# Performance work log

Measured on AMD Instinct MI355X. Metric: run time of the kernel, lower is better.

## Reference

```python
import jax, jax.numpy as jnp
import numpy as np
import math

EPS = 1e-12  # matches F.normalize eps


def _l2_normalize(x):
    # F.normalize(x, p=2, dim=1): x / max(||x||, eps)
    n = jnp.sqrt(jnp.sum(x * x, axis=-1, keepdims=True))
    return x / jnp.maximum(n, EPS)


def setup_inputs() -> dict:
    key = jax.random.key(0)
    k1, k2 = jax.random.split(key)
    B, C, D = 4096, 10000, 1024
    features = jax.random.normal(k1, (B, D), dtype=jnp.float32)
    prototypes = jax.random.normal(k2, (C, D), dtype=jnp.float32)
    distance_scale = jnp.ones((1,), dtype=jnp.float32)
    temperature = jnp.ones((1,), dtype=jnp.float32)
    return {"features": features, "prototypes": prototypes,
            "distance_scale": distance_scale, "temperature": temperature}


def reference(features, prototypes, distance_scale, temperature):
    f = _l2_normalize(features)          # [B, D]
    p = _l2_normalize(prototypes)        # [C, D]
    # ||f - p||^2 = 2 - 2 f.p for unit vectors; clamp tiny negatives from fp error
    sq = jnp.maximum(2.0 - 2.0 * jnp.einsum('bd,cd->bc', f, p), EPS)
    dist = jnp.sqrt(sq) / math.sqrt(2.0)                      # [B, C]
    iso = jnp.abs(distance_scale) * dist                      # [B, C]
    logits = -(iso + jnp.mean(iso, axis=1, keepdims=True))
    return logits / temperature
```

## Files before the change

kernel.cpp:

```cpp
#include <hip/hip_runtime.h>
#include <hip/hip_bf16.h>

typedef __attribute__((ext_vector_type(8))) short short8;
typedef __attribute__((ext_vector_type(4))) float f32x4;

#define GLOBAL_AS __attribute__((address_space(1)))
#define LDS_AS    __attribute__((address_space(3)))

__device__ __forceinline__ void async_ld16(const void* g, void* l) {
    __builtin_amdgcn_global_load_lds((const GLOBAL_AS void*)g, (LDS_AS void*)l, 16, 0, 0);
}

__device__ __forceinline__ unsigned short f2bf(float x) {
    union { __hip_bfloat16 h; unsigned short u; } cv;
    cv.h = __float2bfloat16(x);
    return cv.u;
}

__global__ __launch_bounds__(256) void norm_rows_kernel(
    const float* __restrict__ in, unsigned short* __restrict__ outb, int rows_in)
{
    const int row = blockIdx.x;
    const int tid = threadIdx.x;
    float4 v = make_float4(0.f, 0.f, 0.f, 0.f);
    if (row < rows_in)
        v = reinterpret_cast<const float4*>(in + (size_t)row * 1024)[tid];
    float s = v.x * v.x + v.y * v.y + v.z * v.z + v.w * v.w;
    #pragma unroll
    for (int off = 32; off > 0; off >>= 1) s += __shfl_down(s, off);
    __shared__ float sr[4];
    if ((tid & 63) == 0) sr[tid >> 6] = s;
    __syncthreads();
    const float tot = sr[0] + sr[1] + sr[2] + sr[3];
    const float inv = 1.f / fmaxf(sqrtf(tot), 1e-12f);
    ushort4 o;
    o.x = f2bf(v.x * inv);
    o.y = f2bf(v.y * inv);
    o.z = f2bf(v.z * inv);
    o.w = f2bf(v.w * inv);
    reinterpret_cast<ushort4*>(outb + (size_t)row * 1024)[tid] = o;
}

__global__ __launch_bounds__(256) void zero_f32_kernel(float* __restrict__ p, int n)
{
    const int i = blockIdx.x * 256 + threadIdx.x;
    if (i < n) p[i] = 0.f;
}

__global__ __launch_bounds__(512, 2) void gemm_iso_kernel(
    const unsigned short* __restrict__ A,
    const unsigned short* __restrict__ B,
    float* __restrict__ out,
    float* __restrict__ rowsum,
    const float* __restrict__ ds_ptr,
    int M, int C, int K)
{
    __shared__ __align__(16) char lds[131072];

    const float dsv_raw = ds_ptr[0];

    const int tid  = threadIdx.x;
    const int lane = tid & 63;
    const int wid  = tid >> 6;

    const int nwg  = gridDim.x * gridDim.y;
    const int orig = blockIdx.y * gridDim.x + blockIdx.x;
    const int cpx  = nwg >> 3;
    const int swz  = (orig & 7) * cpx + (orig >> 3);
    const int bx   = swz % gridDim.x;
    const int by   = swz / gridDim.x;
    const int brow = by * 256;
    const int bcol = bx * 256;

    const int lrow8 = lane >> 3;
    const int slotg = (lane & 7) ^ lrow8;
    const size_t kb = (size_t)K * 2;

    const char* pA[4]; const char* pB[4]; int lA[4], lB[4];
    #pragma unroll
    for (int i = 0; i < 4; ++i) {
        const int seg = wid * 4 + i;
        const int r   = seg * 8 + lrow8;
        pA[i] = (const char*)A + (size_t)(brow + r) * kb + slotg * 16;
        pB[i] = (const char*)B + (size_t)(bcol + r) * kb + slotg * 16;
        lA[i] = seg * 1024;
        lB[i] = 32768 + seg * 1024;
    }

    auto STAGE = [&](int buf) {
        char* base = lds + (buf << 16);
        #pragma unroll
        for (int i = 0; i < 4; ++i) async_ld16(pA[i], base + lA[i]);
        #pragma unroll
        for (int i = 0; i < 4; ++i) async_ld16(pB[i], base + lB[i]);
        #pragma unroll
        for (int i = 0; i < 4; ++i) { pA[i] += 128; pB[i] += 128; }
    };

    const int wr = (wid >> 2) * 128;
    const int wc = (wid & 3) * 64;
    const int lr = lane & 15;
    const int kq = lane >> 4;
    const int sx = lr & 7;

    f32x4 acc[8][4];
    #pragma unroll
    for (int m = 0; m < 8; ++m)
        #pragma unroll
        for (int n = 0; n < 4; ++n)
            acc[m][n] = (f32x4){0.f, 0.f, 0.f, 0.f};

    int aoff[8], boff[4];
    #pragma unroll
    for (int m = 0; m < 8; ++m) aoff[m] = (wr + m * 16 + lr) * 128;
    #pragma unroll
    for (int n = 0; n < 4; ++n) boff[n] = 32768 + (wc + n * 16 + lr) * 128;
    const int so0 = ((0 + kq) ^ sx) * 16;
    const int so1 = ((4 + kq) ^ sx) * 16;

    auto COMPUTE = [&](int buf) {
        const char* base = lds + (buf << 16);
        #pragma unroll
        for (int kk = 0; kk < 2; ++kk) {
            const int so = kk ? so1 : so0;
            short8 a[8], b[4];
            #pragma unroll
            for (int m = 0; m < 8; ++m)
                a[m] = *reinterpret_cast<const short8*>(base + aoff[m] + so);
            #pragma unroll
            for (int n = 0; n < 4; ++n)
                b[n] = *reinterpret_cast<const short8*>(base + boff[n] + so);
            __builtin_amdgcn_s_setprio(1);
            #pragma unroll
            for (int m = 0; m < 8; ++m)
                #pragma unroll
                for (int n = 0; n < 4; ++n)
                    acc[m][n] = __builtin_amdgcn_mfma_f32_16x16x32_bf16(
                        a[m], b[n], acc[m][n], 0, 0, 0);
            __builtin_amdgcn_s_setprio(0);
        }
    };

    const int nt = K >> 6;
    STAGE(0);
    STAGE(1);
    asm volatile("s_waitcnt vmcnt(8)" ::: "memory");
    __builtin_amdgcn_s_barrier();
    __builtin_amdgcn_sched_barrier(0);

    for (int t = 0; t < nt; ++t) {
        COMPUTE(t & 1);
        if (t + 1 < nt) {
            __builtin_amdgcn_s_barrier();
            __builtin_amdgcn_sched_barrier(0);
            if (t + 2 < nt) {
                STAGE(t & 1);
                asm volatile("s_waitcnt vmcnt(8)" ::: "memory");
            } else {
                asm volatile("s_waitcnt vmcnt(0)" ::: "memory");
            }
            __builtin_amdgcn_s_barrier();
            __builtin_amdgcn_sched_barrier(0);
        }
    }

    const float dsv = fabsf(dsv_raw);
    #pragma unroll
    for (int m = 0; m < 8; ++m) {
        float rs0 = 0.f, rs1 = 0.f, rs2 = 0.f, rs3 = 0.f;
        const int row0 = brow + wr + m * 16 + kq * 4;
        #pragma unroll
        for (int n = 0; n < 4; ++n) {
            const int col = bcol + wc + n * 16 + lr;
            const bool ok = col < C;
            float* op = out + (size_t)row0 * C + col;
            #pragma unroll
            for (int j = 0; j < 4; ++j) {
                const float sq  = fmaxf(2.f - 2.f * acc[m][n][j], 1e-12f);
                const float iso = dsv * (sqrtf(sq) * 0.70710678118654752f);
                if (ok) op[(size_t)j * C] = iso;
                const float c = ok ? iso : 0.f;
                if (j == 0) rs0 += c; else if (j == 1) rs1 += c;
                else if (j == 2) rs2 += c; else rs3 += c;
            }
        }
        float r4[4] = {rs0, rs1, rs2, rs3};
        #pragma unroll
        for (int j = 0; j < 4; ++j) {
            float r = r4[j];
            r += __shfl_xor(r, 1);
            r += __shfl_xor(r, 2);
            r += __shfl_xor(r, 4);
            r += __shfl_xor(r, 8);
            if (lr == 0) atomicAdd(&rowsum[row0 + j], r);
        }
    }
}

__global__ __launch_bounds__(256) void finalize_kernel(
    float* __restrict__ out, const float* __restrict__ rowsum,
    const float* __restrict__ tptr, int C)
{
    const int row = blockIdx.y;
    const int i4  = blockIdx.x * 256 + threadIdx.x;
    const int n4  = C >> 2;
    if (i4 >= n4) return;
    const float mean = rowsum[row] / (float)C;
    const float invT = 1.f / tptr[0];
    float* rp = out + (size_t)row * C;
    float4 v = reinterpret_cast<const float4*>(rp)[i4];
    v.x = -(v.x + mean) * invT;
    v.y = -(v.y + mean) * invT;
    v.z = -(v.z + mean) * invT;
    v.w = -(v.w + mean) * invT;
    reinterpret_cast<float4*>(rp)[i4] = v;
}

extern "C" void kernel_launch(void* const* d_in, const int* in_sizes, int n_in,
                              void* d_out, int out_size, void* d_ws, size_t ws_size,
                              hipStream_t stream)
{
    const float* feat = (const float*)d_in[0];
    const float* prot = (const float*)d_in[1];
    const float* dsc  = (const float*)d_in[2];
    const float* temp = (const float*)d_in[3];
    float* out = (float*)d_out;

    const int D = 1024;
    const int M = in_sizes[0] / D;
    const int C = in_sizes[1] / D;
    const int NT = (C + 255) / 256;
    const int Npad = NT * 256;

    float* rowsum = (float*)d_ws;
    unsigned short* fbf = (unsigned short*)(rowsum + M);
    unsigned short* pbf = fbf + (size_t)M * D;

    norm_rows_kernel<<<M, 256, 0, stream>>>(feat, fbf, M);
    norm_rows_kernel<<<Npad, 256, 0, stream>>>(prot, pbf, C);
    zero_f32_kernel<<<(M + 255) / 256, 256, 0, stream>>>(rowsum, M);
    gemm_iso_kernel<<<dim3(NT, M / 256), 512, 0, stream>>>(fbf, pbf, out, rowsum, dsc, M, C, D);
    finalize_kernel<<<dim3((C / 4 + 255) / 256, M), 256, 0, stream>>>(out, rowsum, temp, C);
}
```

Before: 386.8 us.

## Restructure GEMM prefetch loop, fuse rowsum zeroing, use row-per-block finalize

Issues the next K-tile's async loads at the start of each iteration, before the current tile's MFMA compute, and waits for all loads before a single barrier. This replaces the earlier two-stage prefetch that needed two barriers per iteration. Rowsum zeroing moves into the feature normalization kernel, removing one launch. The finalize kernel now uses one block per row with a strided loop, giving fewer and larger blocks. The risk is that the new loop keeps only one tile in flight and waits with vmcnt(0) every iteration, so memory latency may be hidden less well.

```diff
diff --git a/kernel.cpp b/kernel.cpp
--- a/kernel.cpp
+++ b/kernel.cpp
@@ -18,10 +18,12 @@
 }
 
 __global__ __launch_bounds__(256) void norm_rows_kernel(
-    const float* __restrict__ in, unsigned short* __restrict__ outb, int rows_in)
+    const float* __restrict__ in, unsigned short* __restrict__ outb, int rows_in,
+    float* __restrict__ rowsum)
 {
     const int row = blockIdx.x;
     const int tid = threadIdx.x;
+    if (rowsum != nullptr && tid == 0) rowsum[row] = 0.f;
     float4 v = make_float4(0.f, 0.f, 0.f, 0.f);
     if (row < rows_in)
         v = reinterpret_cast<const float4*>(in + (size_t)row * 1024)[tid];
@@ -41,12 +43,6 @@
     reinterpret_cast<ushort4*>(outb + (size_t)row * 1024)[tid] = o;
 }
 
-__global__ __launch_bounds__(256) void zero_f32_kernel(float* __restrict__ p, int n)
-{
-    const int i = blockIdx.x * 256 + threadIdx.x;
-    if (i < n) p[i] = 0.f;
-}
-
 __global__ __launch_bounds__(512, 2) void gemm_iso_kernel(
     const unsigned short* __restrict__ A,
     const unsigned short* __restrict__ B,
@@ -63,9 +59,8 @@
     const int lane = tid & 63;
     const int wid  = tid >> 6;
 
-    const int nwg  = gridDim.x * gridDim.y;
     const int orig = blockIdx.y * gridDim.x + blockIdx.x;
-    const int cpx  = nwg >> 3;
+    const int cpx  = (gridDim.x * gridDim.y) >> 3;
     const int swz  = (orig & 7) * cpx + (orig >> 3);
     const int bx   = swz % gridDim.x;
     const int by   = swz / gridDim.x;
@@ -143,22 +138,18 @@
 
     const int nt = K >> 6;
     STAGE(0);
-    STAGE(1);
-    asm volatile("s_waitcnt vmcnt(8)" ::: "memory");
+    asm volatile("s_waitcnt vmcnt(0)" ::: "memory");
     __builtin_amdgcn_s_barrier();
     __builtin_amdgcn_sched_barrier(0);
 
     for (int t = 0; t < nt; ++t) {
+        if (t + 1 < nt) {
+            STAGE((t + 1) & 1);
+            __builtin_amdgcn_sched_barrier(0);
+        }
         COMPUTE(t & 1);
         if (t + 1 < nt) {
-            __builtin_amdgcn_s_barrier();
-            __builtin_amdgcn_sched_barrier(0);
-            if (t + 2 < nt) {
-                STAGE(t & 1);
-                asm volatile("s_waitcnt vmcnt(8)" ::: "memory");
-            } else {
-                asm volatile("s_waitcnt vmcnt(0)" ::: "memory");
-            }
+            asm volatile("s_waitcnt vmcnt(0)" ::: "memory");
             __builtin_amdgcn_s_barrier();
             __builtin_amdgcn_sched_barrier(0);
         }
@@ -201,19 +192,19 @@
     float* __restrict__ out, const float* __restrict__ rowsum,
     const float* __restrict__ tptr, int C)
 {
-    const int row = blockIdx.y;
-    const int i4  = blockIdx.x * 256 + threadIdx.x;
-    const int n4  = C >> 2;
-    if (i4 >= n4) return;
+    const int row = blockIdx.x;
     const float mean = rowsum[row] / (float)C;
     const float invT = 1.f / tptr[0];
     float* rp = out + (size_t)row * C;
-    float4 v = reinterpret_cast<const float4*>(rp)[i4];
-    v.x = -(v.x + mean) * invT;
-    v.y = -(v.y + mean) * invT;
-    v.z = -(v.z + mean) * invT;
-    v.w = -(v.w + mean) * invT;
-    reinterpret_cast<float4*>(rp)[i4] = v;
+    const int n4 = C >> 2;
+    for (int i = threadIdx.x; i < n4; i += 256) {
+        float4 v = reinterpret_cast<const float4*>(rp)[i];
+        v.x = -(v.x + mean) * invT;
+        v.y = -(v.y + mean) * invT;
+        v.z = -(v.z + mean) * invT;
+        v.w = -(v.w + mean) * invT;
+        reinterpret_cast<float4*>(rp)[i] = v;
+    }
 }
 
 extern "C" void kernel_launch(void* const* d_in, const int* in_sizes, int n_in,
@@ -236,9 +227,8 @@
     unsigned short* fbf = (unsigned short*)(rowsum + M);
     unsigned short* pbf = fbf + (size_t)M * D;
 
-    norm_rows_kernel<<<M, 256, 0, stream>>>(feat, fbf, M);
-    norm_rows_kernel<<<Npad, 256, 0, stream>>>(prot, pbf, C);
-    zero_f32_kernel<<<(M + 255) / 256, 256, 0, stream>>>(rowsum, M);
+    norm_rows_kernel<<<M, 256, 0, stream>>>(feat, fbf, M, rowsum);
+    norm_rows_kernel<<<Npad, 256, 0, stream>>>(prot, pbf, C, nullptr);
     gemm_iso_kernel<<<dim3(NT, M / 256), 512, 0, stream>>>(fbf, pbf, out, rowsum, dsc, M, C, D);
-    finalize_kernel<<<dim3((C / 4 + 255) / 256, M), 256, 0, stream>>>(out, rowsum, temp, C);
-}
+    finalize_kernel<<<M, 256, 0, stream>>>(out, rowsum, temp, C);
+}
```

Result: faster. 378.6 us (-2.1%).
